# Optimization experiments

Measured on AMD Instinct MI355X. Metric: run time of the kernel, lower is better.

## Reference

```python
import jax, jax.numpy as jnp
import numpy as np

B, N, K, C_IN, C_ADD, C_MID, C_OUT = 2, 65536, 16, 64, 3, 16, 128
IN_FEATURES = (C_IN + C_ADD) * C_MID  # 1072


def setup_inputs() -> dict:
    key = jax.random.key(0)
    k1, k2, k3, k4, k5, k6 = jax.random.split(key, 6)
    input_feat = jax.random.normal(k1, (B, N, C_IN), dtype=jnp.float32)
    neighbor_inds = jax.random.randint(k2, (B, N, K), 0, N, dtype=jnp.int64)
    weightnet = jax.random.normal(k3, (B, N, K, C_MID), dtype=jnp.float32)
    additional_features = jax.random.normal(k4, (B, N, K, C_ADD), dtype=jnp.float32)
    linear_weight = jax.random.normal(k5, (C_OUT, IN_FEATURES), dtype=jnp.float32) * (1.0 / np.sqrt(IN_FEATURES))
    linear_bias = jax.random.normal(k6, (C_OUT,), dtype=jnp.float32) * 0.01
    return {
        "input_feat": input_feat,
        "neighbor_inds": neighbor_inds,
        "weightnet": weightnet,
        "additional_features": additional_features,
        "linear_weight": linear_weight,
        "linear_bias": linear_bias,
    }


def reference(input_feat, neighbor_inds, weightnet, additional_features, linear_weight, linear_bias):
    # Gather neighbor features: [B, M, K, C_in]
    gathered = jax.vmap(lambda f, idx: f[idx])(input_feat, neighbor_inds)
    # Concat additional per-neighbor features: [B, M, K, C_in + C_add]
    feat = jnp.concatenate([gathered, additional_features], axis=-1)
    # Weighted reduction over K neighbors: [B, M, C_total, C_mid]
    pconv = jnp.einsum('bmkc,bmkj->bmcj', feat, weightnet)
    pconv = pconv.reshape(pconv.shape[0], pconv.shape[1], -1)  # [B, M, C_total*C_mid]
    # Linear layer
    out = jnp.einsum('bmi,oi->bmo', pconv, linear_weight) + linear_bias
    return out
```

## Files before the change

kernel.cpp:

```cpp
#include <hip/hip_runtime.h>
#include <hip/hip_bf16.h>

namespace {
constexpr int NPTS  = 65536;
constexpr int KNB   = 16;
constexpr int CMID  = 16;
constexpr int CIN   = 64;
constexpr int CADD  = 3;
constexpr int COUT  = 128;
constexpr int KREAL = 1072;
constexpr int KPAD  = 1088;
constexpr int MT    = 32;
constexpr int PSTR  = 1092;
constexpr int NKT   = KPAD / 32;
constexpr int NWAVE = 8;
constexpr int TSZ   = 256;
}

typedef __attribute__((ext_vector_type(8))) __bf16 bf16x8;
typedef __attribute__((ext_vector_type(4))) float f32x4;
typedef __attribute__((ext_vector_type(4))) float f32x4v;

union ABFrag { bf16x8 v; uint4 u; };

__device__ __forceinline__ unsigned short bf(float x) {
  __hip_bfloat16 h = __float2bfloat16(x);
  return *reinterpret_cast<unsigned short*>(&h);
}
__device__ __forceinline__ unsigned int pack_bf2(float a, float b) {
  __hip_bfloat162 h = __float22bfloat162_rn(make_float2(a, b));
  return *reinterpret_cast<unsigned int*>(&h);
}

__global__ void convert_w(const float* __restrict__ W, unsigned short* __restrict__ Wb) {
  const int o = blockIdx.x;
  for (int k = threadIdx.x; k < KPAD; k += blockDim.x) {
    float v = (k < KREAL) ? W[o * KREAL + k] : 0.0f;
    Wb[o * KPAD + k] = bf(v);
  }
}

__global__ __launch_bounds__(512, 4) void pconv_fused(
    const float* __restrict__ feat,
    const int* __restrict__ nidx,
    const float* __restrict__ wn,
    const float* __restrict__ addf,
    const float* __restrict__ W,
    const float* __restrict__ bias,
    const unsigned short* __restrict__ Wb,
    int useWb,
    float* __restrict__ out)
{
  __shared__ __align__(16) unsigned short s_p[MT * PSTR];
  __shared__ __align__(16) unsigned short s_x[NWAVE * 2 * TSZ + 16];

  const int tid  = threadIdx.x;
  const int wid  = tid >> 6;
  const int lane = tid & 63;
  const int q    = lane >> 4;
  const int l    = lane & 15;
  const int kq   = lane >> 2;
  const int sub  = lane & 3;

  unsigned short* T0 = s_x + wid * (2 * TSZ);
  unsigned short* T1 = T0 + TSZ;

  {
    const int mg0 = blockIdx.x * MT + wid * 4;
    const int b   = (blockIdx.x * MT) >> 16;
    const float* fb = feat + (size_t)b * (NPTS * CIN);

    int nb[4];
#pragma unroll
    for (int pl = 0; pl < 4; ++pl)
      nb[pl] = __builtin_nontemporal_load(nidx + (size_t)(mg0 + pl) * KNB + kq);

    f32x4v wv[4];
    float  av[4];
#pragma unroll
    for (int pl = 0; pl < 4; ++pl) {
      const int mg = mg0 + pl;
      wv[pl] = __builtin_nontemporal_load(reinterpret_cast<const f32x4v*>(
          wn + (size_t)mg * (KNB * CMID) + kq * CMID + sub * 4));
      av[pl] = 0.f;
      if (sub < CADD)
        av[pl] = __builtin_nontemporal_load(
            addf + (size_t)mg * (KNB * CADD) + kq * CADD + sub);
    }

    f32x4v fvn[4];
    {
      const float* fr = fb + (size_t)nb[0] * CIN + sub * 4;
#pragma unroll
      for (int t = 0; t < 4; ++t)
        fvn[t] = *reinterpret_cast<const f32x4v*>(fr + 16 * t);
    }

    const f32x4 zacc = {0.f, 0.f, 0.f, 0.f};

#pragma unroll
    for (int pl = 0; pl < 4; ++pl) {
      f32x4v fv[4];
#pragma unroll
      for (int t = 0; t < 4; ++t) fv[t] = fvn[t];
      if (pl < 3) {
        const float* fr = fb + (size_t)nb[pl + 1] * CIN + sub * 4;
#pragma unroll
        for (int t = 0; t < 4; ++t)
          fvn[t] = *reinterpret_cast<const f32x4v*>(fr + 16 * t);
      }

      unsigned short* prow = s_p + (wid * 4 + pl) * PSTR;

      T0[(sub * 4 + 0) * 16 + kq] = bf(wv[pl].x);
      T0[(sub * 4 + 1) * 16 + kq] = bf(wv[pl].y);
      T0[(sub * 4 + 2) * 16 + kq] = bf(wv[pl].z);
      T0[(sub * 4 + 3) * 16 + kq] = bf(wv[pl].w);
      {
        unsigned short* d = T1 + (sub * 4) * 16 + kq;
        d[0 * 16] = bf(fv[0].x); d[1 * 16] = bf(fv[0].y);
        d[2 * 16] = bf(fv[0].z); d[3 * 16] = bf(fv[0].w);
      }

      ABFrag fa, fb0;
      fa.u  = make_uint4(0, 0, 0, 0);
      fb0.u = make_uint4(0, 0, 0, 0);
      if (q < 2) {
        fa.v  = *reinterpret_cast<const bf16x8*>(T0 + l * 16 + q * 8);
        fb0.v = *reinterpret_cast<const bf16x8*>(T1 + l * 16 + q * 8);
      }

      {
        unsigned short* d = T0 + (sub * 4) * 16 + kq;
        d[0 * 16] = bf(fv[1].x); d[1 * 16] = bf(fv[1].y);
        d[2 * 16] = bf(fv[1].z); d[3 * 16] = bf(fv[1].w);
      }
      f32x4 d0 = __builtin_amdgcn_mfma_f32_16x16x32_bf16(fa.v, fb0.v, zacc, 0, 0, 0);
      { uint2 w2; w2.x = pack_bf2(d0[0], d0[1]); w2.y = pack_bf2(d0[2], d0[3]);
        *reinterpret_cast<uint2*>(prow + (0 * 16 + l) * 16 + q * 4) = w2; }

      ABFrag fb1; fb1.u = make_uint4(0, 0, 0, 0);
      if (q < 2) fb1.v = *reinterpret_cast<const bf16x8*>(T0 + l * 16 + q * 8);
      {
        unsigned short* d = T1 + (sub * 4) * 16 + kq;
        d[0 * 16] = bf(fv[2].x); d[1 * 16] = bf(fv[2].y);
        d[2 * 16] = bf(fv[2].z); d[3 * 16] = bf(fv[2].w);
      }
      f32x4 d1 = __builtin_amdgcn_mfma_f32_16x16x32_bf16(fa.v, fb1.v, zacc, 0, 0, 0);
      { uint2 w2; w2.x = pack_bf2(d1[0], d1[1]); w2.y = pack_bf2(d1[2], d1[3]);
        *reinterpret_cast<uint2*>(prow + (1 * 16 + l) * 16 + q * 4) = w2; }

      ABFrag fb2; fb2.u = make_uint4(0, 0, 0, 0);
      if (q < 2) fb2.v = *reinterpret_cast<const bf16x8*>(T1 + l * 16 + q * 8);
      {
        unsigned short* d = T0 + (sub * 4) * 16 + kq;
        d[0 * 16] = bf(fv[3].x); d[1 * 16] = bf(fv[3].y);
        d[2 * 16] = bf(fv[3].z); d[3 * 16] = bf(fv[3].w);
      }
      f32x4 d2 = __builtin_amdgcn_mfma_f32_16x16x32_bf16(fa.v, fb2.v, zacc, 0, 0, 0);
      { uint2 w2; w2.x = pack_bf2(d2[0], d2[1]); w2.y = pack_bf2(d2[2], d2[3]);
        *reinterpret_cast<uint2*>(prow + (2 * 16 + l) * 16 + q * 4) = w2; }

      ABFrag fb3; fb3.u = make_uint4(0, 0, 0, 0);
      if (q < 2) fb3.v = *reinterpret_cast<const bf16x8*>(T0 + l * 16 + q * 8);
      {
        if (lane < 52)
          *reinterpret_cast<uint2*>(T1 + (3 + (lane >> 2)) * 16 + (lane & 3) * 4) =
              make_uint2(0u, 0u);
        if (sub < CADD)
          T1[sub * 16 + kq] = bf(av[pl]);
      }
      f32x4 d3 = __builtin_amdgcn_mfma_f32_16x16x32_bf16(fa.v, fb3.v, zacc, 0, 0, 0);
      { uint2 w2; w2.x = pack_bf2(d3[0], d3[1]); w2.y = pack_bf2(d3[2], d3[3]);
        *reinterpret_cast<uint2*>(prow + (3 * 16 + l) * 16 + q * 4) = w2; }

      ABFrag fb4; fb4.u = make_uint4(0, 0, 0, 0);
      if (q < 2) fb4.v = *reinterpret_cast<const bf16x8*>(T1 + l * 16 + q * 8);
      f32x4 d4 = __builtin_amdgcn_mfma_f32_16x16x32_bf16(fa.v, fb4.v, zacc, 0, 0, 0);
      if (l < 4) {
        uint2 w2; w2.x = pack_bf2(d4[0], d4[1]); w2.y = pack_bf2(d4[2], d4[3]);
        *reinterpret_cast<uint2*>(prow + (4 * 16 + l) * 16 + q * 4) = w2;
      }
    }
  }

  __syncthreads();

  const int ob = wid * 16;
  const float bv = bias[ob + l];

  f32x4 acc0 = {0.f, 0.f, 0.f, 0.f};
  f32x4 acc1 = {0.f, 0.f, 0.f, 0.f};

  const unsigned short* wp = Wb + (size_t)(ob + l) * KPAD + q * 8;
  const float* wf = W + (size_t)(ob + l) * KREAL + q * 8;

#pragma unroll 2
  for (int kt = 0; kt < NKT; ++kt) {
    const bf16x8 a0 = *reinterpret_cast<const bf16x8*>(
        s_p + l * PSTR + kt * 32 + q * 8);
    const bf16x8 a1 = *reinterpret_cast<const bf16x8*>(
        s_p + (16 + l) * PSTR + kt * 32 + q * 8);
    ABFrag bb;
    if (useWb) {
      bb.u = *reinterpret_cast<const uint4*>(wp + kt * 32);
    } else {
      const int kb = kt * 32 + q * 8;
      bb.u = make_uint4(0, 0, 0, 0);
      if (kb < KREAL) {
        const float4* s0 = reinterpret_cast<const float4*>(wf + kt * 32);
        const float4 x0 = s0[0], x1 = s0[1];
        bb.u = make_uint4(pack_bf2(x0.x, x0.y), pack_bf2(x0.z, x0.w),
                          pack_bf2(x1.x, x1.y), pack_bf2(x1.z, x1.w));
      }
    }
    acc0 = __builtin_amdgcn_mfma_f32_16x16x32_bf16(a0, bb.v, acc0, 0, 0, 0);
    acc1 = __builtin_amdgcn_mfma_f32_16x16x32_bf16(a1, bb.v, acc1, 0, 0, 0);
  }

  const int m0 = blockIdx.x * MT;
#pragma unroll
  for (int r = 0; r < 4; ++r) {
    __builtin_nontemporal_store(acc0[r] + bv,
        out + (size_t)(m0 + q * 4 + r) * COUT + ob + l);
    __builtin_nontemporal_store(acc1[r] + bv,
        out + (size_t)(m0 + 16 + q * 4 + r) * COUT + ob + l);
  }
}

extern "C" void kernel_launch(void* const* d_in, const int* in_sizes, int n_in,
                              void* d_out, int out_size, void* d_ws, size_t ws_size,
                              hipStream_t stream) {
  const float* feat = (const float*)d_in[0];
  const int*   nidx = (const int*)d_in[1];
  const float* wn   = (const float*)d_in[2];
  const float* addf = (const float*)d_in[3];
  const float* W    = (const float*)d_in[4];
  const float* bias = (const float*)d_in[5];
  float* out = (float*)d_out;

  unsigned short* Wb = (unsigned short*)d_ws;
  const int useWb = (ws_size >= (size_t)COUT * KPAD * 2) ? 1 : 0;
  if (useWb) {
    convert_w<<<COUT, 256, 0, stream>>>(W, Wb);
  }
  const int nblocks = (2 * NPTS) / MT;
  pconv_fused<<<nblocks, 512, 0, stream>>>(feat, nidx, wn, addf, W, bias, Wb, useWb, out);
}
```

Baseline: 399.4 us.

## Halve point tile, XOR-swizzle LDS rows, and software-prefetch weight fragments

Each block now handles 16 points instead of 32, so each wave builds two point rows and runs a single 16x16 MFMA accumulator in the linear stage. The padded LDS row stride is replaced by an XOR swizzle on 16-byte chunks to avoid bank conflicts, and the LDS footprint is roughly halved so more blocks can be resident (launch bounds raised to 6). The bf16 weight fragments are loaded into a 4-deep register ring ahead of use to hide global latency. The trade-off is that each weight fragment loaded from global/L2 now feeds only 16 points instead of 32, doubling weight traffic per point.

```diff
diff --git a/kernel.cpp b/kernel.cpp
--- a/kernel.cpp
+++ b/kernel.cpp
@@ -10,11 +10,12 @@
 constexpr int COUT  = 128;
 constexpr int KREAL = 1072;
 constexpr int KPAD  = 1088;
-constexpr int MT    = 32;
-constexpr int PSTR  = 1092;
+constexpr int MT    = 16;
+constexpr int ROWB  = KPAD * 2;
 constexpr int NKT   = KPAD / 32;
 constexpr int NWAVE = 8;
 constexpr int TSZ   = 256;
+constexpr int PF    = 4;
 }
 
 typedef __attribute__((ext_vector_type(8))) __bf16 bf16x8;
@@ -40,7 +41,7 @@
   }
 }
 
-__global__ __launch_bounds__(512, 4) void pconv_fused(
+__global__ __launch_bounds__(512, 6) void pconv_fused(
     const float* __restrict__ feat,
     const int* __restrict__ nidx,
     const float* __restrict__ wn,
@@ -51,8 +52,10 @@
     int useWb,
     float* __restrict__ out)
 {
-  __shared__ __align__(16) unsigned short s_p[MT * PSTR];
+  __shared__ __align__(16) unsigned short s_p[MT * KPAD];
   __shared__ __align__(16) unsigned short s_x[NWAVE * 2 * TSZ + 16];
+
+  char* s_pb = reinterpret_cast<char*>(s_p);
 
   const int tid  = threadIdx.x;
   const int wid  = tid >> 6;
@@ -66,19 +69,19 @@
   unsigned short* T1 = T0 + TSZ;
 
   {
-    const int mg0 = blockIdx.x * MT + wid * 4;
+    const int mg0 = blockIdx.x * MT + wid * 2;
     const int b   = (blockIdx.x * MT) >> 16;
     const float* fb = feat + (size_t)b * (NPTS * CIN);
 
-    int nb[4];
-#pragma unroll
-    for (int pl = 0; pl < 4; ++pl)
+    int nb[2];
+#pragma unroll
+    for (int pl = 0; pl < 2; ++pl)
       nb[pl] = __builtin_nontemporal_load(nidx + (size_t)(mg0 + pl) * KNB + kq);
 
-    f32x4v wv[4];
-    float  av[4];
-#pragma unroll
-    for (int pl = 0; pl < 4; ++pl) {
+    f32x4v wv[2];
+    float  av[2];
+#pragma unroll
+    for (int pl = 0; pl < 2; ++pl) {
       const int mg = mg0 + pl;
       wv[pl] = __builtin_nontemporal_load(reinterpret_cast<const f32x4v*>(
           wn + (size_t)mg * (KNB * CMID) + kq * CMID + sub * 4));
@@ -99,18 +102,20 @@
     const f32x4 zacc = {0.f, 0.f, 0.f, 0.f};
 
 #pragma unroll
-    for (int pl = 0; pl < 4; ++pl) {
+    for (int pl = 0; pl < 2; ++pl) {
       f32x4v fv[4];
 #pragma unroll
       for (int t = 0; t < 4; ++t) fv[t] = fvn[t];
-      if (pl < 3) {
+      if (pl < 1) {
         const float* fr = fb + (size_t)nb[pl + 1] * CIN + sub * 4;
 #pragma unroll
         for (int t = 0; t < 4; ++t)
           fvn[t] = *reinterpret_cast<const f32x4v*>(fr + 16 * t);
       }
 
-      unsigned short* prow = s_p + (wid * 4 + pl) * PSTR;
+      const int p = wid * 2 + pl;
+      char* prow = s_pb + p * ROWB;
+      const int rsw = (p & 7) << 4;
 
       T0[(sub * 4 + 0) * 16 + kq] = bf(wv[pl].x);
       T0[(sub * 4 + 1) * 16 + kq] = bf(wv[pl].y);
@@ -137,7 +142,7 @@
       }
       f32x4 d0 = __builtin_amdgcn_mfma_f32_16x16x32_bf16(fa.v, fb0.v, zacc, 0, 0, 0);
       { uint2 w2; w2.x = pack_bf2(d0[0], d0[1]); w2.y = pack_bf2(d0[2], d0[3]);
-        *reinterpret_cast<uint2*>(prow + (0 * 16 + l) * 16 + q * 4) = w2; }
+        *reinterpret_cast<uint2*>(prow + (((0 * 16 + l) * 32 + q * 8) ^ rsw)) = w2; }
 
       ABFrag fb1; fb1.u = make_uint4(0, 0, 0, 0);
       if (q < 2) fb1.v = *reinterpret_cast<const bf16x8*>(T0 + l * 16 + q * 8);
@@ -148,7 +153,7 @@
       }
       f32x4 d1 = __builtin_amdgcn_mfma_f32_16x16x32_bf16(fa.v, fb1.v, zacc, 0, 0, 0);
       { uint2 w2; w2.x = pack_bf2(d1[0], d1[1]); w2.y = pack_bf2(d1[2], d1[3]);
-        *reinterpret_cast<uint2*>(prow + (1 * 16 + l) * 16 + q * 4) = w2; }
+        *reinterpret_cast<uint2*>(prow + (((1 * 16 + l) * 32 + q * 8) ^ rsw)) = w2; }
 
       ABFrag fb2; fb2.u = make_uint4(0, 0, 0, 0);
       if (q < 2) fb2.v = *reinterpret_cast<const bf16x8*>(T1 + l * 16 + q * 8);
@@ -159,7 +164,7 @@
       }
       f32x4 d2 = __builtin_amdgcn_mfma_f32_16x16x32_bf16(fa.v, fb2.v, zacc, 0, 0, 0);
       { uint2 w2; w2.x = pack_bf2(d2[0], d2[1]); w2.y = pack_bf2(d2[2], d2[3]);
-        *reinterpret_cast<uint2*>(prow + (2 * 16 + l) * 16 + q * 4) = w2; }
+        *reinterpret_cast<uint2*>(prow + (((2 * 16 + l) * 32 + q * 8) ^ rsw)) = w2; }
 
       ABFrag fb3; fb3.u = make_uint4(0, 0, 0, 0);
       if (q < 2) fb3.v = *reinterpret_cast<const bf16x8*>(T0 + l * 16 + q * 8);
@@ -172,14 +177,14 @@
       }
       f32x4 d3 = __builtin_amdgcn_mfma_f32_16x16x32_bf16(fa.v, fb3.v, zacc, 0, 0, 0);
       { uint2 w2; w2.x = pack_bf2(d3[0], d3[1]); w2.y = pack_bf2(d3[2], d3[3]);
-        *reinterpret_cast<uint2*>(prow + (3 * 16 + l) * 16 + q * 4) = w2; }
+        *reinterpret_cast<uint2*>(prow + (((3 * 16 + l) * 32 + q * 8) ^ rsw)) = w2; }
 
       ABFrag fb4; fb4.u = make_uint4(0, 0, 0, 0);
       if (q < 2) fb4.v = *reinterpret_cast<const bf16x8*>(T1 + l * 16 + q * 8);
       f32x4 d4 = __builtin_amdgcn_mfma_f32_16x16x32_bf16(fa.v, fb4.v, zacc, 0, 0, 0);
       if (l < 4) {
         uint2 w2; w2.x = pack_bf2(d4[0], d4[1]); w2.y = pack_bf2(d4[2], d4[3]);
-        *reinterpret_cast<uint2*>(prow + (4 * 16 + l) * 16 + q * 4) = w2;
+        *reinterpret_cast<uint2*>(prow + (((4 * 16 + l) * 32 + q * 8) ^ rsw)) = w2;
       }
     }
   }
@@ -189,23 +194,33 @@
   const int ob = wid * 16;
   const float bv = bias[ob + l];
 
-  f32x4 acc0 = {0.f, 0.f, 0.f, 0.f};
-  f32x4 acc1 = {0.f, 0.f, 0.f, 0.f};
+  f32x4 acc = {0.f, 0.f, 0.f, 0.f};
 
   const unsigned short* wp = Wb + (size_t)(ob + l) * KPAD + q * 8;
   const float* wf = W + (size_t)(ob + l) * KREAL + q * 8;
-
+  const int asw = (l & 7) << 4;
+
+  if (useWb) {
+    ABFrag wb[PF];
+#pragma unroll
+    for (int i = 0; i < PF; ++i)
+      wb[i].u = *reinterpret_cast<const uint4*>(wp + i * 32);
+#pragma unroll
+    for (int kt = 0; kt < NKT; ++kt) {
+      ABFrag cur = wb[kt & (PF - 1)];
+      if (kt + PF < NKT)
+        wb[kt & (PF - 1)].u = *reinterpret_cast<const uint4*>(wp + (kt + PF) * 32);
+      const bf16x8 a = *reinterpret_cast<const bf16x8*>(
+          s_pb + l * ROWB + ((kt * 64 + q * 16) ^ asw));
+      acc = __builtin_amdgcn_mfma_f32_16x16x32_bf16(a, cur.v, acc, 0, 0, 0);
+    }
+  } else {
 #pragma unroll 2
-  for (int kt = 0; kt < NKT; ++kt) {
-    const bf16x8 a0 = *reinterpret_cast<const bf16x8*>(
-        s_p + l * PSTR + kt * 32 + q * 8);
-    const bf16x8 a1 = *reinterpret_cast<const bf16x8*>(
-        s_p + (16 + l) * PSTR + kt * 32 + q * 8);
-    ABFrag bb;
-    if (useWb) {
-      bb.u = *reinterpret_cast<const uint4*>(wp + kt * 32);
-    } else {
+    for (int kt = 0; kt < NKT; ++kt) {
+      const bf16x8 a = *reinterpret_cast<const bf16x8*>(
+          s_pb + l * ROWB + ((kt * 64 + q * 16) ^ asw));
       const int kb = kt * 32 + q * 8;
+      ABFrag bb;
       bb.u = make_uint4(0, 0, 0, 0);
       if (kb < KREAL) {
         const float4* s0 = reinterpret_cast<const float4*>(wf + kt * 32);
@@ -213,19 +228,15 @@
         bb.u = make_uint4(pack_bf2(x0.x, x0.y), pack_bf2(x0.z, x0.w),
                           pack_bf2(x1.x, x1.y), pack_bf2(x1.z, x1.w));
       }
-    }
-    acc0 = __builtin_amdgcn_mfma_f32_16x16x32_bf16(a0, bb.v, acc0, 0, 0, 0);
-    acc1 = __builtin_amdgcn_mfma_f32_16x16x32_bf16(a1, bb.v, acc1, 0, 0, 0);
+      acc = __builtin_amdgcn_mfma_f32_16x16x32_bf16(a, bb.v, acc, 0, 0, 0);
+    }
   }
 
   const int m0 = blockIdx.x * MT;
 #pragma unroll
-  for (int r = 0; r < 4; ++r) {
-    __builtin_nontemporal_store(acc0[r] + bv,
+  for (int r = 0; r < 4; ++r)
+    __builtin_nontemporal_store(acc[r] + bv,
         out + (size_t)(m0 + q * 4 + r) * COUT + ob + l);
-    __builtin_nontemporal_store(acc1[r] + bv,
-        out + (size_t)(m0 + 16 + q * 4 + r) * COUT + ob + l);
-  }
 }
 
 extern "C" void kernel_launch(void* const* d_in, const int* in_sizes, int n_in,
```

Result: slower. 499.8 us (+25.1%).
